# Kernel tuning notes

Hardware: AMD Instinct MI355X
Metric: run time of the kernel (lower is better)

Reference implementation:

```python
import jax, jax.numpy as jnp
import numpy as np


def setup_inputs() -> dict:
    key = jax.random.key(0)
    kK, kV, kQ, kP, kA = jax.random.split(key, 5)
    b, d, N, T = 16, 512, 1024, 2048
    K = jax.random.normal(kK, (b, d, N), dtype=jnp.float32)
    V = jax.random.normal(kV, (b, d, N), dtype=jnp.float32)
    Q = jax.random.normal(kQ, (b, d, T), dtype=jnp.float32)
    previous_position = jax.random.randint(kP, (b,), 0, N)
    # previous attention: a valid attention matrix (softmax over N)
    previous_att = jax.nn.softmax(jax.random.uniform(kA, (b, N, T), dtype=jnp.float32), axis=1)
    return {
        "K": K,
        "V": V,
        "Q": Q,
        "force_incremental": 1,   # static python int -> bool branch
        "previous_position": previous_position,
        "previous_att": previous_att,
        "current_time": 1024,     # static python int timestep
    }


def reference(K, V, Q, force_incremental, previous_position, previous_att, current_time):
    # K, V: [b, d, N]; Q: [b, d, T]
    d = Q.shape[1]
    scale = 1.0 / np.sqrt(d)  # Config.d == feature dim
    # A: [b, N, T], softmax over N (text axis)
    A = jax.nn.softmax(jnp.einsum('bdn,bdt->bnt', K, Q) * scale, axis=1)
    current_position = jnp.argmax(A[:, :, current_time], axis=1)  # [b]
    if force_incremental:
        N = A.shape[1]
        # restore already-committed alignment prefix
        A = A.at[:, :, :current_time].set(previous_att[:, :, :current_time])
        difference = current_position - previous_position
        force_needed = (difference < -1) | (difference > 3)  # [b]
        # delta: one-hot at previous_position+1 (scatter_ of ones collapses to one-hot)
        idx = jnp.clip(previous_position + 1, 0, N - 1)
        delta = jax.nn.one_hot(idx, N, dtype=A.dtype)  # [b, N]
        col = jnp.where(force_needed[:, None], delta, A[:, :, current_time])
        A = A.at[:, :, current_time].set(col)
        current_position = jnp.argmax(col, axis=1)
    # R: [b, d, T]
    R = jnp.einsum('bdn,bnt->bdt', V, A)
    return A, R, current_position
```

## Files before the change

kernel.cpp:

```cpp
#include <hip/hip_runtime.h>
#include <hip/hip_bf16.h>

#define B_  16
#define D_  512
#define N_  1024
#define T_  2048
#define CT_ 1024
#define SCALE 0.04419417382415922f

typedef __attribute__((ext_vector_type(8))) short bf16x8;
typedef __attribute__((ext_vector_type(4))) float f32x4;
typedef __attribute__((ext_vector_type(8))) unsigned short u16x8;

#define GLDS16(g, l) __builtin_amdgcn_global_load_lds( \
    (const __attribute__((address_space(1))) unsigned int*)(g), \
    (__attribute__((address_space(3))) unsigned int*)(l), 16, 0, 0)

__device__ __forceinline__ unsigned short f2bf(float f) {
    union { float f; unsigned u; } v; v.f = f;
    unsigned r = v.u + 0x7fffu + ((v.u >> 16) & 1u);
    return (unsigned short)(r >> 16);
}
__device__ __forceinline__ float bf2f(unsigned short s) {
    union { unsigned u; float f; } v; v.u = ((unsigned)s) << 16;
    return v.f;
}


__global__ __launch_bounds__(256) void prep_all(
    const float* __restrict__ K, const float* __restrict__ Q,
    const float* __restrict__ V, const float* __restrict__ prev_att,
    unsigned short* __restrict__ KT, unsigned short* __restrict__ QT,
    unsigned short* __restrict__ Vbf, float* __restrict__ A,
    unsigned short* __restrict__ PbfT, float* __restrict__ invsum,
    float* __restrict__ colS_part) {
    __shared__ float tl[64][65];
    __shared__ float qv_s[64];
    __shared__ float red[256];
    const int bid = blockIdx.x;
    const int tid = threadIdx.x;
    const int rr = tid >> 4, cc = (tid & 15) * 4;

    if (bid < 4096) {
        const int nx = bid & 15, rem = bid >> 4;
        const int ty_ = rem & 15, b = rem >> 4;
        const int n0 = nx * 64, t0 = ty_ * 64;
        const float* ib = prev_att + (long)b * N_ * T_;
        float* Ab = A + (long)b * N_ * T_;
        unsigned short* ob = PbfT + (long)b * T_ * N_;
        f32x4 v[4];
#pragma unroll
        for (int p = 0; p < 4; ++p)
            v[p] = __builtin_nontemporal_load(
                (const f32x4*)&ib[(long)(n0 + p * 16 + rr) * T_ + t0 + cc]);
#pragma unroll
        for (int p = 0; p < 4; ++p)
            __builtin_nontemporal_store(
                v[p], (f32x4*)&Ab[(long)(n0 + p * 16 + rr) * T_ + t0 + cc]);
#pragma unroll
        for (int p = 0; p < 4; ++p) {
            tl[p*16+rr][cc] = v[p][0]; tl[p*16+rr][cc+1] = v[p][1];
            tl[p*16+rr][cc+2] = v[p][2]; tl[p*16+rr][cc+3] = v[p][3];
        }
        __syncthreads();
#pragma unroll
        for (int p = 0; p < 4; ++p) {
            int c = p * 16 + rr;
            ushort4 w;
            w.x = f2bf(tl[cc+0][c]); w.y = f2bf(tl[cc+1][c]);
            w.z = f2bf(tl[cc+2][c]); w.w = f2bf(tl[cc+3][c]);
            *(ushort4*)&ob[(long)(t0 + c) * N_ + n0 + cc] = w;
        }
    } else if (bid < 6144) {
        const int r = bid - 4096;
        const int rx = r & 7, rem = r >> 3;
        const int cy = rem & 15, b = rem >> 4;
        const int r0 = rx * 64, c0 = cy * 64;
        const float* ib = K + (long)b * D_ * N_;
        unsigned short* ob = KT + (long)b * 1024 * 512;
        if (tid < 64)
            qv_s[tid] = __builtin_nontemporal_load(
                &Q[((long)b * D_ + r0 + tid) * T_ + CT_]);
        f32x4 v[4];
#pragma unroll
        for (int p = 0; p < 4; ++p)
            v[p] = __builtin_nontemporal_load(
                (const f32x4*)&ib[(long)(r0 + p * 16 + rr) * N_ + c0 + cc]);
#pragma unroll
        for (int p = 0; p < 4; ++p) {
            tl[p*16+rr][cc] = v[p][0]; tl[p*16+rr][cc+1] = v[p][1];
            tl[p*16+rr][cc+2] = v[p][2]; tl[p*16+rr][cc+3] = v[p][3];
        }
        __syncthreads();
#pragma unroll
        for (int p = 0; p < 4; ++p) {
            int c = p * 16 + rr;
            ushort4 w;
            w.x = f2bf(tl[cc+0][c]); w.y = f2bf(tl[cc+1][c]);
            w.z = f2bf(tl[cc+2][c]); w.w = f2bf(tl[cc+3][c]);
            *(ushort4*)&ob[(long)(c0 + c) * 512 + r0 + cc] = w;
        }
        {
            const int n = tid & 63, g = tid >> 6;
            float p = 0.f;
#pragma unroll
            for (int j = 0; j < 16; ++j)
                p += tl[g * 16 + j][n] * qv_s[g * 16 + j];
            red[tid] = p;
            __syncthreads();
            if (tid < 64)
                colS_part[((long)b * 8 + rx) * 1024 + c0 + tid] =
                    red[tid] + red[64 + tid] + red[128 + tid] + red[192 + tid];
        }
    } else if (bid < 8192) {
        const int r = bid - 6144;
        const int rx = r & 7, rem = r >> 3;
        const int cy = rem & 15, b = rem >> 4;
        const int r0 = rx * 64, c0 = cy * 64;
        const float* ib = Q + (long)b * D_ * T_;
        unsigned short* ob = QT + (long)b * 1024 * 512;
        f32x4 v[4];
#pragma unroll
        for (int p = 0; p < 4; ++p)
            v[p] = __builtin_nontemporal_load(
                (const f32x4*)&ib[(long)(r0 + p * 16 + rr) * T_ + CT_ + c0 + cc]);
#pragma unroll
        for (int p = 0; p < 4; ++p) {
            tl[p*16+rr][cc] = v[p][0]; tl[p*16+rr][cc+1] = v[p][1];
            tl[p*16+rr][cc+2] = v[p][2]; tl[p*16+rr][cc+3] = v[p][3];
        }
        __syncthreads();
#pragma unroll
        for (int p = 0; p < 4; ++p) {
            int c = p * 16 + rr;
            ushort4 w;
            w.x = f2bf(tl[cc+0][c]); w.y = f2bf(tl[cc+1][c]);
            w.z = f2bf(tl[cc+2][c]); w.w = f2bf(tl[cc+3][c]);
            *(ushort4*)&ob[(long)(c0 + c) * 512 + r0 + cc] = w;
        }
    } else if (bid < 9216) {
        const long total = (long)B_ * D_ * N_ / 4;
        for (long i = (long)(bid - 8192) * 256 + tid; i < total; i += 1024L * 256) {
            f32x4 v = __builtin_nontemporal_load(&((const f32x4*)V)[i]);
            ushort4 w;
            w.x = f2bf(v[0]); w.y = f2bf(v[1]); w.z = f2bf(v[2]); w.w = f2bf(v[3]);
            ((ushort4*)Vbf)[i] = w;
        }
    } else {
        const int idx = (bid - 9216) * 256 + tid;
        const int b = idx >> 10, t = idx & 1023;
        invsum[(long)b * T_ + t] = 1.0f;
    }
}

__global__ __launch_bounds__(256) void score_gemm_fused(
    const unsigned short* __restrict__ KT, const unsigned short* __restrict__ QT,
    unsigned short* __restrict__ PbfT, float* __restrict__ partial) {
    const int wg = blockIdx.x;
    const int b  = wg >> 6;
    const int rem = wg & 63;
    const int by = rem >> 3;
    const int bx = rem & 7;
    const int m0 = by * 128;
    const int t0 = bx * 128;
    __shared__ __align__(16) unsigned short buf[128 * 136];
    __shared__ float csum[2][128];
    unsigned short* sA = buf;
    unsigned short* sB = buf + 128 * 64;
    const int tid = threadIdx.x, lane = tid & 63, wave = tid >> 6;
    const int wm = wave >> 1, wn = wave & 1;
    const int lq = lane & 15, half = lane >> 4;
    const int srow = tid >> 3;
    const int cin  = tid & 7;

    const unsigned short* Ab = KT + (long)b * N_ * 512;
    const unsigned short* Bb = QT + (long)b * N_ * 512;

    f32x4 acc[4][4];
#pragma unroll
    for (int i = 0; i < 4; ++i)
#pragma unroll
        for (int j = 0; j < 4; ++j) acc[i][j] = f32x4{0.f, 0.f, 0.f, 0.f};

    for (int k0 = 0; k0 < 512; k0 += 64) {
#pragma unroll
        for (int c = 0; c < 4; ++c) {
            const int row  = c * 32 + srow;
            const int clog = cin ^ (row & 7);
            GLDS16(Ab + (long)(m0 + row) * 512 + k0 + clog * 8,
                   &sA[(c * 256 + wave * 64) * 8]);
            GLDS16(Bb + (long)(t0 + row) * 512 + k0 + clog * 8,
                   &sB[(c * 256 + wave * 64) * 8]);
        }
        __syncthreads();
#pragma unroll
        for (int kk = 0; kk < 2; ++kk) {
            bf16x8 af[4], bfr[4];
#pragma unroll
            for (int mi = 0; mi < 4; ++mi) {
                const int row = wm * 64 + mi * 16 + lq;
                af[mi] = *(const bf16x8*)&sA[row * 64 + (((kk * 4 + half) ^ (row & 7)) * 8)];
            }
#pragma unroll
            for (int ni = 0; ni < 4; ++ni) {
                const int row = wn * 64 + ni * 16 + lq;
                bfr[ni] = *(const bf16x8*)&sB[row * 64 + (((kk * 4 + half) ^ (row & 7)) * 8)];
            }
#pragma unroll
            for (int mi = 0; mi < 4; ++mi)
#pragma unroll
                for (int ni = 0; ni < 4; ++ni)
                    acc[mi][ni] = __builtin_amdgcn_mfma_f32_16x16x32_bf16(
                        af[mi], bfr[ni], acc[mi][ni], 0, 0, 0);
        }
        __syncthreads();
    }

#pragma unroll
    for (int mi = 0; mi < 4; ++mi)
#pragma unroll
        for (int ni = 0; ni < 4; ++ni)
#pragma unroll
            for (int r = 0; r < 4; ++r)
                acc[mi][ni][r] = __expf(acc[mi][ni][r] * SCALE);

    float cp[4];
#pragma unroll
    for (int ni = 0; ni < 4; ++ni) {
        float s = 0.f;
#pragma unroll
        for (int mi = 0; mi < 4; ++mi)
#pragma unroll
            for (int r = 0; r < 4; ++r) s += acc[mi][ni][r];
        s += __shfl_xor(s, 16);
        s += __shfl_xor(s, 32);
        cp[ni] = s;
    }

#pragma unroll
    for (int mi = 0; mi < 4; ++mi)
#pragma unroll
        for (int ni = 0; ni < 4; ++ni) {
            const int col = wn * 64 + ni * 16 + lq;
            const int row = wm * 64 + mi * 16 + half * 4;
            ushort4 w;
            w.x = f2bf(acc[mi][ni][0]); w.y = f2bf(acc[mi][ni][1]);
            w.z = f2bf(acc[mi][ni][2]); w.w = f2bf(acc[mi][ni][3]);
            *(ushort4*)&buf[col * 136 + row] = w;
        }
    if (lane < 16) {
#pragma unroll
        for (int ni = 0; ni < 4; ++ni)
            csum[wm][wn * 64 + ni * 16 + lane] = cp[ni];
    }
    __syncthreads();

    if (tid < 128)
        partial[((long)b * 8 + by) * 1024 + t0 + tid] =
            csum[0][tid] + csum[1][tid];

    unsigned short* ob = PbfT + (long)b * T_ * N_;
#pragma unroll
    for (int p = 0; p < 8; ++p) {
        const int idx = tid + p * 256;
        const int row = idx >> 4, ch = idx & 15;
        u16x8 w = *(const u16x8*)&buf[row * 136 + ch * 8];
        *(u16x8*)&ob[(long)(CT_ + t0 + row) * N_ + m0 + ch * 8] = w;
    }
}

__global__ void finalize_all(float* __restrict__ A, unsigned short* __restrict__ PbfT,
                             float* __restrict__ invsum,
                             const float* __restrict__ colS_part,
                             const float* __restrict__ partial,
                             float* __restrict__ pos_out,
                             const int* __restrict__ prev_pos,
                             const int* __restrict__ force_p) {
    const int force = *force_p;
    const int b = blockIdx.x;
    const int tid = threadIdx.x;
    float* Ab = A + (long)b * N_ * T_;
    __shared__ float s[N_];
    __shared__ float redf[256];
    __shared__ int   redi[256];

    for (int t = tid; t < 1024; t += 256) {
        float sm = 0.f;
#pragma unroll
        for (int k = 0; k < 8; ++k) sm += partial[((long)b * 8 + k) * 1024 + t];
        invsum[(long)b * T_ + CT_ + t] = 1.f / sm;
    }

    for (int n = tid; n < N_; n += 256) {
        float v = 0.f;
#pragma unroll
        for (int k = 0; k < 8; ++k) v += colS_part[((long)b * 8 + k) * 1024 + n];
        s[n] = v * SCALE;
    }
    __syncthreads();

    float m = -1e30f;
    for (int n = tid; n < N_; n += 256) m = fmaxf(m, s[n]);
    redf[tid] = m; __syncthreads();
    for (int w = 128; w > 0; w >>= 1) {
        if (tid < w) redf[tid] = fmaxf(redf[tid], redf[tid + w]);
        __syncthreads();
    }
    m = redf[0];
    __syncthreads();

    float sum = 0.f;
    for (int n = tid; n < N_; n += 256) sum += __expf(s[n] - m);
    redf[tid] = sum; __syncthreads();
    for (int w = 128; w > 0; w >>= 1) {
        if (tid < w) redf[tid] += redf[tid + w];
        __syncthreads();
    }
    sum = redf[0];
    __syncthreads();

    int idxl = N_;
    for (int n = tid; n < N_; n += 256) if (s[n] == m && n < idxl) idxl = n;
    redi[tid] = idxl; __syncthreads();
    for (int w = 128; w > 0; w >>= 1) {
        if (tid < w) redi[tid] = min(redi[tid], redi[tid + w]);
        __syncthreads();
    }
    const int cpos = redi[0];

    const int prev = prev_pos[b];
    const int diff = cpos - prev;
    const int fneed = force && (diff < -1 || diff > 3);
    int oneidx = prev + 1;
    oneidx = oneidx < 0 ? 0 : (oneidx > N_ - 1 ? N_ - 1 : oneidx);
    const float inv = 1.f / sum;

    for (int n = tid; n < N_; n += 256) {
        float v = fneed ? (n == oneidx ? 1.f : 0.f) : __expf(s[n] - m) * inv;
        Ab[(long)n * T_ + CT_] = v;
        PbfT[(long)b * T_ * N_ + (long)CT_ * N_ + n] = f2bf(v);
    }
    if (tid == 0) {
        invsum[(long)b * T_ + CT_] = 1.0f;
        pos_out[b] = (float)(fneed ? oneidx : cpos);
    }
}

__global__ __launch_bounds__(256) void rgemm_emitA(
    const unsigned short* __restrict__ Vbf, const unsigned short* __restrict__ PbfT,
    const float* __restrict__ invsum, float* __restrict__ R, float* __restrict__ A) {
    __shared__ __align__(16) unsigned char smem[33792];
    const int tid = threadIdx.x;

    if (blockIdx.x < 1024) {
        unsigned short* sA = (unsigned short*)smem;
        unsigned short* sB = (unsigned short*)(smem + 16384);
        const int wg = blockIdx.x;
        const int b  = wg >> 6;
        const int rem = wg & 63;
        const int by = rem >> 4;
        const int bx = rem & 15;
        const int m0  = by * 128;
        const int nn0 = bx * 128;
        const int lane = tid & 63, wave = tid >> 6;
        const int wm = wave >> 1, wn = wave & 1;
        const int lq = lane & 15, half = lane >> 4;
        const int srow = tid >> 3;
        const int cin  = tid & 7;

        const unsigned short* Ab = Vbf  + (long)b * D_ * N_;
        const unsigned short* Bb = PbfT + (long)b * T_ * N_;

        f32x4 acc[4][4];
#pragma unroll
        for (int i = 0; i < 4; ++i)
#pragma unroll
            for (int j = 0; j < 4; ++j) acc[i][j] = f32x4{0.f, 0.f, 0.f, 0.f};

        for (int k0 = 0; k0 < 1024; k0 += 64) {
#pragma unroll
            for (int c = 0; c < 4; ++c) {
                const int row  = c * 32 + srow;
                const int clog = cin ^ (row & 7);
                GLDS16(Ab + (long)(m0  + row) * 1024 + k0 + clog * 8,
                       &sA[(c * 256 + wave * 64) * 8]);
                GLDS16(Bb + (long)(nn0 + row) * 1024 + k0 + clog * 8,
                       &sB[(c * 256 + wave * 64) * 8]);
            }
            __syncthreads();
#pragma unroll
            for (int kk = 0; kk < 2; ++kk) {
                bf16x8 af[4], bfr[4];
#pragma unroll
                for (int mi = 0; mi < 4; ++mi) {
                    const int row = wm * 64 + mi * 16 + lq;
                    af[mi] = *(const bf16x8*)&sA[row * 64 + (((kk * 4 + half) ^ (row & 7)) * 8)];
                }
#pragma unroll
                for (int ni = 0; ni < 4; ++ni) {
                    const int row = wn * 64 + ni * 16 + lq;
                    bfr[ni] = *(const bf16x8*)&sB[row * 64 + (((kk * 4 + half) ^ (row & 7)) * 8)];
                }
#pragma unroll
                for (int mi = 0; mi < 4; ++mi)
#pragma unroll
                    for (int ni = 0; ni < 4; ++ni)
                        acc[mi][ni] = __builtin_amdgcn_mfma_f32_16x16x32_bf16(
                            af[mi], bfr[ni], acc[mi][ni], 0, 0, 0);
            }
            __syncthreads();
        }
        float* Rb = R + (long)b * D_ * T_;
#pragma unroll
        for (int ni = 0; ni < 4; ++ni) {
            const int col = nn0 + wn * 64 + ni * 16 + lq;
            const float inv = invsum[(long)b * T_ + col];
#pragma unroll
            for (int mi = 0; mi < 4; ++mi)
#pragma unroll
                for (int r = 0; r < 4; ++r) {
                    const int row = m0 + wm * 64 + mi * 16 + half * 4 + r;
                    __builtin_nontemporal_store(acc[mi][ni][r] * inv,
                                                &Rb[(long)row * T_ + col]);
                }
        }
    } else {
        float (*tl)[65] = (float(*)[65])smem;
        float* inv_s = (float*)(smem + 33280);
        const int r = blockIdx.x - 1024;
        const int n0x = r & 15, rem = r >> 4;
        const int tcy = rem & 7, b = rem >> 3;
        const int n0  = n0x * 64;
        const int tc0 = tcy * 128;
        if (tid < 128) inv_s[tid] = invsum[(long)b * T_ + CT_ + tc0 + tid];
        __syncthreads();
        const unsigned short* Pb = PbfT + (long)b * T_ * N_;
        float* Ab = A + (long)b * N_ * T_;
        const int rr = tid >> 4, cc = (tid & 15) * 4;
#pragma unroll
        for (int p = 0; p < 8; ++p) {
            const int row = p * 16 + rr;
            ushort4 w = *(const ushort4*)&Pb[(long)(CT_ + tc0 + row) * N_ + n0 + cc];
            const float inv = inv_s[row];
            tl[row][cc]   = bf2f(w.x) * inv; tl[row][cc+1] = bf2f(w.y) * inv;
            tl[row][cc+2] = bf2f(w.z) * inv; tl[row][cc+3] = bf2f(w.w) * inv;
        }
        __syncthreads();
        const int rr2 = tid >> 5, cc2 = (tid & 31) * 4;
#pragma unroll
        for (int p = 0; p < 8; ++p) {
            const int c = p * 8 + rr2;
            f32x4 o;
            o[0] = tl[cc2+0][c]; o[1] = tl[cc2+1][c];
            o[2] = tl[cc2+2][c]; o[3] = tl[cc2+3][c];
            __builtin_nontemporal_store(
                o, (f32x4*)&Ab[(long)(n0 + c) * T_ + CT_ + tc0 + cc2]);
        }
    }
}

__global__ void copy_prefix(const float* __restrict__ prev_att, float* __restrict__ A) {
    const int per_row = CT_ >> 2;
    const long total = (long)B_ * N_ * per_row;
    for (long i = (long)blockIdx.x * blockDim.x + threadIdx.x; i < total;
         i += (long)gridDim.x * blockDim.x) {
        long row = i / per_row;
        int  c4  = (int)(i - row * per_row);
        long off = row * T_ + (long)c4 * 4;
        *(float4*)(A + off) = *(const float4*)(prev_att + off);
    }
}

__global__ void softmax_part_old(const float* __restrict__ A, float* __restrict__ partial) {
    const int b  = blockIdx.z;
    const int n0 = blockIdx.y * 128;
    const int tx = threadIdx.x & 63, ty = threadIdx.x >> 6;
    const int ci = blockIdx.x * 64 + tx;
    const int t  = CT_ + ci;
    const float* Ab = A + (long)b * N_ * T_;
    float s = 0.f;
    for (int r = ty; r < 128; r += 4)
        s += __expf(Ab[(long)(n0 + r) * T_ + t] * SCALE);
    __shared__ float red2[4][64];
    red2[ty][tx] = s;
    __syncthreads();
    if (ty == 0) {
        float tot = red2[0][tx] + red2[1][tx] + red2[2][tx] + red2[3][tx];
        partial[((long)b * 8 + blockIdx.y) * 1024 + ci] = tot;
    }
}

__global__ __launch_bounds__(256) void score_gemm_old(
    const float* __restrict__ K, const float* __restrict__ Q, float* __restrict__ A) {
    const int b  = blockIdx.z;
    const int n0 = blockIdx.y * 128;
    const int t0 = blockIdx.x * 128;
    __shared__ __align__(16) unsigned short sK[128 * 40];
    __shared__ __align__(16) unsigned short sQ[128 * 40];
    const int tid = threadIdx.x;
    const int lane = tid & 63, wave = tid >> 6;
    const int wm = wave >> 1, wn = wave & 1;
    const int lq = lane & 15, half = lane >> 4;
    const int xl = tid & 127, grp = tid >> 7;
    f32x4 acc[4][4];
#pragma unroll
    for (int i = 0; i < 4; ++i)
#pragma unroll
        for (int j = 0; j < 4; ++j) acc[i][j] = f32x4{0.f, 0.f, 0.f, 0.f};
    const float* Kb = K + (long)b * D_ * N_;
    const float* Qb = Q + (long)b * D_ * T_;
    for (int d0 = 0; d0 < D_; d0 += 32) {
#pragma unroll
        for (int j = 0; j < 4; ++j) {
            ushort4 w;
#pragma unroll
            for (int i = 0; i < 4; ++i)
                ((unsigned short*)&w)[i] = f2bf(Kb[(long)(d0 + grp*16 + j*4 + i) * N_ + n0 + xl]);
            *(ushort4*)&sK[xl * 40 + grp * 16 + j * 4] = w;
        }
#pragma unroll
        for (int j = 0; j < 4; ++j) {
            ushort4 w;
#pragma unroll
            for (int i = 0; i < 4; ++i)
                ((unsigned short*)&w)[i] = f2bf(Qb[(long)(d0 + grp*16 + j*4 + i) * T_ + CT_ + t0 + xl]);
            *(ushort4*)&sQ[xl * 40 + grp * 16 + j * 4] = w;
        }
        __syncthreads();
        bf16x8 af[4], bfr[4];
#pragma unroll
        for (int mi = 0; mi < 4; ++mi)
            af[mi] = *(const bf16x8*)&sK[(wm * 64 + mi * 16 + lq) * 40 + half * 8];
#pragma unroll
        for (int ni = 0; ni < 4; ++ni)
            bfr[ni] = *(const bf16x8*)&sQ[(wn * 64 + ni * 16 + lq) * 40 + half * 8];
#pragma unroll
        for (int mi = 0; mi < 4; ++mi)
#pragma unroll
            for (int ni = 0; ni < 4; ++ni)
                acc[mi][ni] = __builtin_amdgcn_mfma_f32_16x16x32_bf16(
                    af[mi], bfr[ni], acc[mi][ni], 0, 0, 0);
        __syncthreads();
    }
    float* Ab = A + (long)b * N_ * T_;
#pragma unroll
    for (int mi = 0; mi < 4; ++mi)
#pragma unroll
        for (int ni = 0; ni < 4; ++ni) {
            const int col = CT_ + t0 + wn * 64 + ni * 16 + lq;
#pragma unroll
            for (int r = 0; r < 4; ++r)
                Ab[(long)(n0 + wm*64 + mi*16 + half*4 + r) * T_ + col] = acc[mi][ni][r];
        }
}

__global__ void softmax_scale_old(float* __restrict__ A, const float* __restrict__ partial) {
    const int b  = blockIdx.z;
    const int n0 = blockIdx.y * 256;
    const int tx = threadIdx.x & 63, ty = threadIdx.x >> 6;
    const int ci = blockIdx.x * 64 + tx;
    const int t  = CT_ + ci;
    float sum = 0.f;
#pragma unroll
    for (int k = 0; k < 8; ++k) sum += partial[((long)b * 8 + k) * 1024 + ci];
    const float inv = 1.f / sum;
    float* Ab = A + (long)b * N_ * T_;
    for (int r = ty; r < 256; r += 4) {
        long off = (long)(n0 + r) * T_ + t;
        Ab[off] = __expf(Ab[off] * SCALE) * inv;
    }
}

__global__ void col_scores_fp32(const float* __restrict__ K, const float* __restrict__ Q,
                                float* __restrict__ A) {
    const int b  = blockIdx.y;
    const int n0 = blockIdx.x * 128;
    const int tid = threadIdx.x;
    const int nl = tid & 127, dh = tid >> 7;
    __shared__ float qv[D_];
    __shared__ float part[256];
    for (int d = tid; d < D_; d += 256) qv[d] = Q[((long)b * D_ + d) * T_ + CT_];
    __syncthreads();
    float acc = 0.f;
    const float* Kb = K + (long)b * D_ * N_;
    for (int d = dh * 256; d < dh * 256 + 256; ++d)
        acc += Kb[(long)d * N_ + n0 + nl] * qv[d];
    part[tid] = acc;
    __syncthreads();
    if (tid < 128) {
        float s = (part[tid] + part[tid + 128]) * SCALE;
        A[((long)b * N_ + n0 + nl) * T_ + CT_] = s;
    }
}

__global__ void finalize_col_old(float* __restrict__ A, float* __restrict__ pos_out,
                                 const int* __restrict__ prev_pos,
                                 const int* __restrict__ force_p) {
    const int force = *force_p;
    const int b = blockIdx.x;
    const int tid = threadIdx.x;
    float* Ab = A + (long)b * N_ * T_;
    __shared__ float s[N_];
    __shared__ float redf[256];
    __shared__ int   redi[256];

    for (int n = tid; n < N_; n += 256) s[n] = Ab[(long)n * T_ + CT_];
    __syncthreads();
    float m = -1e30f;
    for (int n = tid; n < N_; n += 256) m = fmaxf(m, s[n]);
    redf[tid] = m; __syncthreads();
    for (int w = 128; w > 0; w >>= 1) {
        if (tid < w) redf[tid] = fmaxf(redf[tid], redf[tid + w]);
        __syncthreads();
    }
    m = redf[0];
    __syncthreads();
    float sum = 0.f;
    for (int n = tid; n < N_; n += 256) sum += __expf(s[n] - m);
    redf[tid] = sum; __syncthreads();
    for (int w = 128; w > 0; w >>= 1) {
        if (tid < w) redf[tid] += redf[tid + w];
        __syncthreads();
    }
    sum = redf[0];
    __syncthreads();
    int idxl = N_;
    for (int n = tid; n < N_; n += 256) if (s[n] == m && n < idxl) idxl = n;
    redi[tid] = idxl; __syncthreads();
    for (int w = 128; w > 0; w >>= 1) {
        if (tid < w) redi[tid] = min(redi[tid], redi[tid + w]);
        __syncthreads();
    }
    const int cpos = redi[0];
    const int prev = prev_pos[b];
    const int diff = cpos - prev;
    const int fneed = force && (diff < -1 || diff > 3);
    int oneidx = prev + 1;
    oneidx = oneidx < 0 ? 0 : (oneidx > N_ - 1 ? N_ - 1 : oneidx);
    const float inv = 1.f / sum;
    for (int n = tid; n < N_; n += 256) {
        float v = fneed ? (n == oneidx ? 1.f : 0.f) : __expf(s[n] - m) * inv;
        Ab[(long)n * T_ + CT_] = v;
    }
    if (tid == 0) pos_out[b] = (float)(fneed ? oneidx : cpos);
}

__global__ __launch_bounds__(256) void r_gemm_old(
    const float* __restrict__ V, const float* __restrict__ A, float* __restrict__ R) {
    const int b  = blockIdx.z;
    const int d0 = blockIdx.y * 128;
    const int t0 = blockIdx.x * 128;
    __shared__ __align__(16) unsigned short sV[128 * 40];
    __shared__ __align__(16) unsigned short sA2[128 * 40];
    const int tid = threadIdx.x;
    const int lane = tid & 63, wave = tid >> 6;
    const int wm = wave >> 1, wn = wave & 1;
    const int lq = lane & 15, half = lane >> 4;
    const int xl = tid & 127, grp = tid >> 7;
    const int vd = tid >> 3, vn4 = (tid & 7) * 4;
    f32x4 acc[4][4];
#pragma unroll
    for (int i = 0; i < 4; ++i)
#pragma unroll
        for (int j = 0; j < 4; ++j) acc[i][j] = f32x4{0.f, 0.f, 0.f, 0.f};
    const float* Vb = V + (long)b * D_ * N_;
    const float* Ab = A + (long)b * N_ * T_;
    for (int n0 = 0; n0 < N_; n0 += 32) {
#pragma unroll
        for (int p = 0; p < 4; ++p) {
            int dl = p * 32 + vd;
            float4 v = *(const float4*)&Vb[(long)(d0 + dl) * N_ + n0 + vn4];
            ushort4 w;
            w.x = f2bf(v.x); w.y = f2bf(v.y); w.z = f2bf(v.z); w.w = f2bf(v.w);
            *(ushort4*)&sV[dl * 40 + vn4] = w;
        }
#pragma unroll
        for (int j = 0; j < 4; ++j) {
            ushort4 w;
#pragma unroll
            for (int i = 0; i < 4; ++i)
                ((unsigned short*)&w)[i] = f2bf(Ab[(long)(n0 + grp*16 + j*4 + i) * T_ + t0 + xl]);
            *(ushort4*)&sA2[xl * 40 + grp * 16 + j * 4] = w;
        }
        __syncthreads();
        bf16x8 af[4], bfr[4];
#pragma unroll
        for (int mi = 0; mi < 4; ++mi)
            af[mi] = *(const bf16x8*)&sV[(wm * 64 + mi * 16 + lq) * 40 + half * 8];
#pragma unroll
        for (int ni = 0; ni < 4; ++ni)
            bfr[ni] = *(const bf16x8*)&sA2[(wn * 64 + ni * 16 + lq) * 40 + half * 8];
#pragma unroll
        for (int mi = 0; mi < 4; ++mi)
#pragma unroll
            for (int ni = 0; ni < 4; ++ni)
                acc[mi][ni] = __builtin_amdgcn_mfma_f32_16x16x32_bf16(
                    af[mi], bfr[ni], acc[mi][ni], 0, 0, 0);
        __syncthreads();
    }
    float* Rb = R + (long)b * D_ * T_;
#pragma unroll
    for (int mi = 0; mi < 4; ++mi)
#pragma unroll
        for (int ni = 0; ni < 4; ++ni) {
            const int col = t0 + wn * 64 + ni * 16 + lq;
#pragma unroll
            for (int r = 0; r < 4; ++r)
                Rb[(long)(d0 + wm*64 + mi*16 + half*4 + r) * T_ + col] = acc[mi][ni][r];
        }
}

extern "C" void kernel_launch(void* const* d_in, const int* in_sizes, int n_in,
                              void* d_out, int out_size, void* d_ws, size_t ws_size,
                              hipStream_t stream) {
    const float* K        = (const float*)d_in[0];
    const float* V        = (const float*)d_in[1];
    const float* Q        = (const float*)d_in[2];
    const int*   force_p  = (const int*)d_in[3];
    const int*   prev_pos = (const int*)d_in[4];
    const float* prev_att = (const float*)d_in[5];

    float* A       = (float*)d_out;
    float* R       = A + (long)B_ * N_ * T_;
    float* pos_out = R + (long)B_ * D_ * T_;

    const size_t oKT = 0;
    const size_t oQT = oKT + (size_t)B_ * N_ * D_ * 2;
    const size_t oV  = oQT + (size_t)B_ * N_ * D_ * 2;
    const size_t oPT = oV  + (size_t)B_ * D_ * N_ * 2;
    const size_t oP  = oPT + (size_t)B_ * T_ * N_ * 2;
    const size_t oI  = oP  + (size_t)B_ * 8 * 1024 * 4;
    const size_t oCP = oI  + (size_t)B_ * T_ * 4;
    const size_t need = oCP + (size_t)B_ * 8 * 1024 * 4;

    float* partial = (float*)((char*)d_ws + (ws_size >= need ? oP : 0));

    if (ws_size >= need) {
        unsigned short* KT   = (unsigned short*)((char*)d_ws + oKT);
        unsigned short* QT   = (unsigned short*)((char*)d_ws + oQT);
        unsigned short* Vbf  = (unsigned short*)((char*)d_ws + oV);
        unsigned short* PbfT = (unsigned short*)((char*)d_ws + oPT);
        float*          invs = (float*)((char*)d_ws + oI);
        float*          colP = (float*)((char*)d_ws + oCP);

        prep_all        <<<9280, 256, 0, stream>>>(K, Q, V, prev_att,
                                                   KT, QT, Vbf, A, PbfT, invs, colP);
        score_gemm_fused<<<1024, 256, 0, stream>>>(KT, QT, PbfT, partial);
        finalize_all    <<<B_, 256, 0, stream>>>(A, PbfT, invs, colP, partial,
                                                 pos_out, prev_pos, force_p);
        rgemm_emitA     <<<3072, 256, 0, stream>>>(Vbf, PbfT, invs, R, A);
    } else {
        copy_prefix       <<<2048, 256, 0, stream>>>(prev_att, A);
        score_gemm_old    <<<dim3(8, 8, B_), 256, 0, stream>>>(K, Q, A);
        softmax_part_old  <<<dim3(16, 8, B_), 256, 0, stream>>>(A, partial);
        softmax_scale_old <<<dim3(16, 4, B_), 256, 0, stream>>>(A, partial);
        col_scores_fp32   <<<dim3(8, B_), 256, 0, stream>>>(K, Q, A);
        finalize_col_old  <<<B_, 256, 0, stream>>>(A, pos_out, prev_pos, force_p);
        r_gemm_old        <<<dim3(16, 4, B_), 256, 0, stream>>>(V, A, R);
    }
}
```

Measured before the change: 164.5 us.

## Interleave score GEMM blocks with prefix copy and V conversion in one launch

Moves the previous-attention prefix copy/transposition and the V-to-bf16 conversion out of the prep kernel and into the score GEMM launch. Every sixth block does the GEMM and the rest do the memory-bound copy work, so compute-heavy and bandwidth-heavy blocks can run on the GPU at the same time. The prep kernel is reduced to the K/Q transpose and init. The cost is more shared memory per block for the copy blocks (sized for the GEMM) and possible contention on memory bandwidth while the GEMM blocks are running.

New measurement: 179.6 us. 9.2% more time.

```diff
diff --git a/kernel.cpp b/kernel.cpp
--- a/kernel.cpp
+++ b/kernel.cpp
@@ -27,13 +27,10 @@
 }
 
 
-__global__ __launch_bounds__(256) void prep_all(
+__global__ __launch_bounds__(256) void prep_kq(
     const float* __restrict__ K, const float* __restrict__ Q,
-    const float* __restrict__ V, const float* __restrict__ prev_att,
     unsigned short* __restrict__ KT, unsigned short* __restrict__ QT,
-    unsigned short* __restrict__ Vbf, float* __restrict__ A,
-    unsigned short* __restrict__ PbfT, float* __restrict__ invsum,
-    float* __restrict__ colS_part) {
+    float* __restrict__ invsum, float* __restrict__ colS_part) {
     __shared__ float tl[64][65];
     __shared__ float qv_s[64];
     __shared__ float red[256];
@@ -41,39 +38,8 @@
     const int tid = threadIdx.x;
     const int rr = tid >> 4, cc = (tid & 15) * 4;
 
-    if (bid < 4096) {
-        const int nx = bid & 15, rem = bid >> 4;
-        const int ty_ = rem & 15, b = rem >> 4;
-        const int n0 = nx * 64, t0 = ty_ * 64;
-        const float* ib = prev_att + (long)b * N_ * T_;
-        float* Ab = A + (long)b * N_ * T_;
-        unsigned short* ob = PbfT + (long)b * T_ * N_;
-        f32x4 v[4];
-#pragma unroll
-        for (int p = 0; p < 4; ++p)
-            v[p] = __builtin_nontemporal_load(
-                (const f32x4*)&ib[(long)(n0 + p * 16 + rr) * T_ + t0 + cc]);
-#pragma unroll
-        for (int p = 0; p < 4; ++p)
-            __builtin_nontemporal_store(
-                v[p], (f32x4*)&Ab[(long)(n0 + p * 16 + rr) * T_ + t0 + cc]);
-#pragma unroll
-        for (int p = 0; p < 4; ++p) {
-            tl[p*16+rr][cc] = v[p][0]; tl[p*16+rr][cc+1] = v[p][1];
-            tl[p*16+rr][cc+2] = v[p][2]; tl[p*16+rr][cc+3] = v[p][3];
-        }
-        __syncthreads();
-#pragma unroll
-        for (int p = 0; p < 4; ++p) {
-            int c = p * 16 + rr;
-            ushort4 w;
-            w.x = f2bf(tl[cc+0][c]); w.y = f2bf(tl[cc+1][c]);
-            w.z = f2bf(tl[cc+2][c]); w.w = f2bf(tl[cc+3][c]);
-            *(ushort4*)&ob[(long)(t0 + c) * N_ + n0 + cc] = w;
-        }
-    } else if (bid < 6144) {
-        const int r = bid - 4096;
-        const int rx = r & 7, rem = r >> 3;
+    if (bid < 2048) {
+        const int rx = bid & 7, rem = bid >> 3;
         const int cy = rem & 15, b = rem >> 4;
         const int r0 = rx * 64, c0 = cy * 64;
         const float* ib = K + (long)b * D_ * N_;
@@ -112,8 +78,8 @@
                 colS_part[((long)b * 8 + rx) * 1024 + c0 + tid] =
                     red[tid] + red[64 + tid] + red[128 + tid] + red[192 + tid];
         }
-    } else if (bid < 8192) {
-        const int r = bid - 6144;
+    } else if (bid < 4096) {
+        const int r = bid - 2048;
         const int rx = r & 7, rem = r >> 3;
         const int cy = rem & 15, b = rem >> 4;
         const int r0 = rx * 64, c0 = cy * 64;
@@ -138,134 +104,177 @@
             w.z = f2bf(tl[cc+2][c]); w.w = f2bf(tl[cc+3][c]);
             *(ushort4*)&ob[(long)(c0 + c) * 512 + r0 + cc] = w;
         }
-    } else if (bid < 9216) {
-        const long total = (long)B_ * D_ * N_ / 4;
-        for (long i = (long)(bid - 8192) * 256 + tid; i < total; i += 1024L * 256) {
-            f32x4 v = __builtin_nontemporal_load(&((const f32x4*)V)[i]);
-            ushort4 w;
-            w.x = f2bf(v[0]); w.y = f2bf(v[1]); w.z = f2bf(v[2]); w.w = f2bf(v[3]);
-            ((ushort4*)Vbf)[i] = w;
-        }
     } else {
-        const int idx = (bid - 9216) * 256 + tid;
+        const int idx = (bid - 4096) * 256 + tid;
         const int b = idx >> 10, t = idx & 1023;
         invsum[(long)b * T_ + t] = 1.0f;
     }
 }
 
-__global__ __launch_bounds__(256) void score_gemm_fused(
+__global__ __launch_bounds__(256) void score_prefix_v(
     const unsigned short* __restrict__ KT, const unsigned short* __restrict__ QT,
-    unsigned short* __restrict__ PbfT, float* __restrict__ partial) {
-    const int wg = blockIdx.x;
-    const int b  = wg >> 6;
-    const int rem = wg & 63;
-    const int by = rem >> 3;
-    const int bx = rem & 7;
-    const int m0 = by * 128;
-    const int t0 = bx * 128;
-    __shared__ __align__(16) unsigned short buf[128 * 136];
-    __shared__ float csum[2][128];
-    unsigned short* sA = buf;
-    unsigned short* sB = buf + 128 * 64;
-    const int tid = threadIdx.x, lane = tid & 63, wave = tid >> 6;
-    const int wm = wave >> 1, wn = wave & 1;
-    const int lq = lane & 15, half = lane >> 4;
-    const int srow = tid >> 3;
-    const int cin  = tid & 7;
-
-    const unsigned short* Ab = KT + (long)b * N_ * 512;
-    const unsigned short* Bb = QT + (long)b * N_ * 512;
-
-    f32x4 acc[4][4];
-#pragma unroll
-    for (int i = 0; i < 4; ++i)
-#pragma unroll
-        for (int j = 0; j < 4; ++j) acc[i][j] = f32x4{0.f, 0.f, 0.f, 0.f};
-
-    for (int k0 = 0; k0 < 512; k0 += 64) {
-#pragma unroll
-        for (int c = 0; c < 4; ++c) {
-            const int row  = c * 32 + srow;
-            const int clog = cin ^ (row & 7);
-            GLDS16(Ab + (long)(m0 + row) * 512 + k0 + clog * 8,
-                   &sA[(c * 256 + wave * 64) * 8]);
-            GLDS16(Bb + (long)(t0 + row) * 512 + k0 + clog * 8,
-                   &sB[(c * 256 + wave * 64) * 8]);
-        }
-        __syncthreads();
-#pragma unroll
-        for (int kk = 0; kk < 2; ++kk) {
-            bf16x8 af[4], bfr[4];
-#pragma unroll
-            for (int mi = 0; mi < 4; ++mi) {
-                const int row = wm * 64 + mi * 16 + lq;
-                af[mi] = *(const bf16x8*)&sA[row * 64 + (((kk * 4 + half) ^ (row & 7)) * 8)];
+    const float* __restrict__ prev_att, const float* __restrict__ V,
+    unsigned short* __restrict__ PbfT, float* __restrict__ partial,
+    float* __restrict__ A, unsigned short* __restrict__ Vbf) {
+    __shared__ __align__(16) unsigned char smem[35840];
+    const int bid = blockIdx.x;
+    const int tid = threadIdx.x;
+
+    if (bid % 6 == 0) {
+        unsigned short* buf = (unsigned short*)smem;
+        float (*csum)[128]  = (float(*)[128])(smem + 34816);
+        unsigned short* sA = buf;
+        unsigned short* sB = buf + 128 * 64;
+        const int wg = bid / 6;
+        const int b  = wg >> 6;
+        const int rem = wg & 63;
+        const int by = rem >> 3;
+        const int bx = rem & 7;
+        const int m0 = by * 128;
+        const int t0 = bx * 128;
+        const int lane = tid & 63, wave = tid >> 6;
+        const int wm = wave >> 1, wn = wave & 1;
+        const int lq = lane & 15, half = lane >> 4;
+        const int srow = tid >> 3;
+        const int cin  = tid & 7;
+
+        const unsigned short* Ab = KT + (long)b * N_ * 512;
+        const unsigned short* Bb = QT + (long)b * N_ * 512;
+
+        f32x4 acc[4][4];
+#pragma unroll
+        for (int i = 0; i < 4; ++i)
+#pragma unroll
+            for (int j = 0; j < 4; ++j) acc[i][j] = f32x4{0.f, 0.f, 0.f, 0.f};
+
+        for (int k0 = 0; k0 < 512; k0 += 64) {
+#pragma unroll
+            for (int c = 0; c < 4; ++c) {
+                const int row  = c * 32 + srow;
+                const int clog = cin ^ (row & 7);
+                GLDS16(Ab + (long)(m0 + row) * 512 + k0 + clog * 8,
+                       &sA[(c * 256 + wave * 64) * 8]);
+                GLDS16(Bb + (long)(t0 + row) * 512 + k0 + clog * 8,
+                       &sB[(c * 256 + wave * 64) * 8]);
             }
+            __syncthreads();
+#pragma unroll
+            for (int kk = 0; kk < 2; ++kk) {
+                bf16x8 af[4], bfr[4];
+#pragma unroll
+                for (int mi = 0; mi < 4; ++mi) {
+                    const int row = wm * 64 + mi * 16 + lq;
+                    af[mi] = *(const bf16x8*)&sA[row * 64 + (((kk * 4 + half) ^ (row & 7)) * 8)];
+                }
+#pragma unroll
+                for (int ni = 0; ni < 4; ++ni) {
+                    const int row = wn * 64 + ni * 16 + lq;
+                    bfr[ni] = *(const bf16x8*)&sB[row * 64 + (((kk * 4 + half) ^ (row & 7)) * 8)];
+                }
+#pragma unroll
+                for (int mi = 0; mi < 4; ++mi)
+#pragma unroll
+                    for (int ni = 0; ni < 4; ++ni)
+                        acc[mi][ni] = __builtin_amdgcn_mfma_f32_16x16x32_bf16(
+                            af[mi], bfr[ni], acc[mi][ni], 0, 0, 0);
+            }
+            __syncthreads();
+        }
+
+#pragma unroll
+        for (int mi = 0; mi < 4; ++mi)
+#pragma unroll
+            for (int ni = 0; ni < 4; ++ni)
+#pragma unroll
+                for (int r = 0; r < 4; ++r)
+                    acc[mi][ni][r] = __expf(acc[mi][ni][r] * SCALE);
+
+        float cp[4];
+#pragma unroll
+        for (int ni = 0; ni < 4; ++ni) {
+            float s = 0.f;
+#pragma unroll
+            for (int mi = 0; mi < 4; ++mi)
+#pragma unroll
+                for (int r = 0; r < 4; ++r) s += acc[mi][ni][r];
+            s += __shfl_xor(s, 16);
+            s += __shfl_xor(s, 32);
+            cp[ni] = s;
+        }
+
+#pragma unroll
+        for (int mi = 0; mi < 4; ++mi)
 #pragma unroll
             for (int ni = 0; ni < 4; ++ni) {
-                const int row = wn * 64 + ni * 16 + lq;
-                bfr[ni] = *(const bf16x8*)&sB[row * 64 + (((kk * 4 + half) ^ (row & 7)) * 8)];
+                const int col = wn * 64 + ni * 16 + lq;
+                const int row = wm * 64 + mi * 16 + half * 4;
+                ushort4 w;
+                w.x = f2bf(acc[mi][ni][0]); w.y = f2bf(acc[mi][ni][1]);
+                w.z = f2bf(acc[mi][ni][2]); w.w = f2bf(acc[mi][ni][3]);
+                *(ushort4*)&buf[col * 136 + row] = w;
             }
-#pragma unroll
-            for (int mi = 0; mi < 4; ++mi)
-#pragma unroll
-                for (int ni = 0; ni < 4; ++ni)
-                    acc[mi][ni] = __builtin_amdgcn_mfma_f32_16x16x32_bf16(
-                        af[mi], bfr[ni], acc[mi][ni], 0, 0, 0);
-        }
-        __syncthreads();
-    }
-
-#pragma unroll
-    for (int mi = 0; mi < 4; ++mi)
-#pragma unroll
-        for (int ni = 0; ni < 4; ++ni)
-#pragma unroll
-            for (int r = 0; r < 4; ++r)
-                acc[mi][ni][r] = __expf(acc[mi][ni][r] * SCALE);
-
-    float cp[4];
-#pragma unroll
-    for (int ni = 0; ni < 4; ++ni) {
-        float s = 0.f;
-#pragma unroll
-        for (int mi = 0; mi < 4; ++mi)
-#pragma unroll
-            for (int r = 0; r < 4; ++r) s += acc[mi][ni][r];
-        s += __shfl_xor(s, 16);
-        s += __shfl_xor(s, 32);
-        cp[ni] = s;
-    }
-
-#pragma unroll
-    for (int mi = 0; mi < 4; ++mi)
-#pragma unroll
-        for (int ni = 0; ni < 4; ++ni) {
-            const int col = wn * 64 + ni * 16 + lq;
-            const int row = wm * 64 + mi * 16 + half * 4;
-            ushort4 w;
-            w.x = f2bf(acc[mi][ni][0]); w.y = f2bf(acc[mi][ni][1]);
-            w.z = f2bf(acc[mi][ni][2]); w.w = f2bf(acc[mi][ni][3]);
-            *(ushort4*)&buf[col * 136 + row] = w;
-        }
-    if (lane < 16) {
-#pragma unroll
-        for (int ni = 0; ni < 4; ++ni)
-            csum[wm][wn * 64 + ni * 16 + lane] = cp[ni];
-    }
-    __syncthreads();
-
-    if (tid < 128)
-        partial[((long)b * 8 + by) * 1024 + t0 + tid] =
-            csum[0][tid] + csum[1][tid];
-
-    unsigned short* ob = PbfT + (long)b * T_ * N_;
-#pragma unroll
-    for (int p = 0; p < 8; ++p) {
-        const int idx = tid + p * 256;
-        const int row = idx >> 4, ch = idx & 15;
-        u16x8 w = *(const u16x8*)&buf[row * 136 + ch * 8];
-        *(u16x8*)&ob[(long)(CT_ + t0 + row) * N_ + m0 + ch * 8] = w;
+        if (lane < 16) {
+#pragma unroll
+            for (int ni = 0; ni < 4; ++ni)
+                csum[wm][wn * 64 + ni * 16 + lane] = cp[ni];
+        }
+        __syncthreads();
+
+        if (tid < 128)
+            partial[((long)b * 8 + by) * 1024 + t0 + tid] =
+                csum[0][tid] + csum[1][tid];
+
+        unsigned short* ob = PbfT + (long)b * T_ * N_;
+#pragma unroll
+        for (int p = 0; p < 8; ++p) {
+            const int idx = tid + p * 256;
+            const int row = idx >> 4, ch = idx & 15;
+            u16x8 w = *(const u16x8*)&buf[row * 136 + ch * 8];
+            *(u16x8*)&ob[(long)(CT_ + t0 + row) * N_ + m0 + ch * 8] = w;
+        }
+    } else {
+        const int oid = bid - bid / 6 - 1;
+        if (oid < 4096) {
+            float (*tl)[65] = (float(*)[65])smem;
+            const int rr = tid >> 4, cc = (tid & 15) * 4;
+            const int nx = oid & 15, rem = oid >> 4;
+            const int ty_ = rem & 15, b = rem >> 4;
+            const int n0 = nx * 64, t0 = ty_ * 64;
+            const float* ib = prev_att + (long)b * N_ * T_;
+            float* Ab = A + (long)b * N_ * T_;
+            unsigned short* ob = PbfT + (long)b * T_ * N_;
+            f32x4 v[4];
+#pragma unroll
+            for (int p = 0; p < 4; ++p)
+                v[p] = __builtin_nontemporal_load(
+                    (const f32x4*)&ib[(long)(n0 + p * 16 + rr) * T_ + t0 + cc]);
+#pragma unroll
+            for (int p = 0; p < 4; ++p)
+                __builtin_nontemporal_store(
+                    v[p], (f32x4*)&Ab[(long)(n0 + p * 16 + rr) * T_ + t0 + cc]);
+#pragma unroll
+            for (int p = 0; p < 4; ++p) {
+                tl[p*16+rr][cc] = v[p][0]; tl[p*16+rr][cc+1] = v[p][1];
+                tl[p*16+rr][cc+2] = v[p][2]; tl[p*16+rr][cc+3] = v[p][3];
+            }
+            __syncthreads();
+#pragma unroll
+            for (int p = 0; p < 4; ++p) {
+                int c = p * 16 + rr;
+                ushort4 w;
+                w.x = f2bf(tl[cc+0][c]); w.y = f2bf(tl[cc+1][c]);
+                w.z = f2bf(tl[cc+2][c]); w.w = f2bf(tl[cc+3][c]);
+                *(ushort4*)&ob[(long)(t0 + c) * N_ + n0 + cc] = w;
+            }
+        } else {
+            const long total = (long)B_ * D_ * N_ / 4;
+            for (long i = (long)(oid - 4096) * 256 + tid; i < total; i += 1024L * 256) {
+                f32x4 v = __builtin_nontemporal_load(&((const f32x4*)V)[i]);
+                ushort4 w;
+                w.x = f2bf(v[0]); w.y = f2bf(v[1]); w.z = f2bf(v[2]); w.w = f2bf(v[3]);
+                ((ushort4*)Vbf)[i] = w;
+            }
+        }
     }
 }
 
@@ -743,12 +752,12 @@
         float*          invs = (float*)((char*)d_ws + oI);
         float*          colP = (float*)((char*)d_ws + oCP);
 
-        prep_all        <<<9280, 256, 0, stream>>>(K, Q, V, prev_att,
-                                                   KT, QT, Vbf, A, PbfT, invs, colP);
-        score_gemm_fused<<<1024, 256, 0, stream>>>(KT, QT, PbfT, partial);
-        finalize_all    <<<B_, 256, 0, stream>>>(A, PbfT, invs, colP, partial,
-                                                 pos_out, prev_pos, force_p);
-        rgemm_emitA     <<<3072, 256, 0, stream>>>(Vbf, PbfT, invs, R, A);
+        prep_kq        <<<4160, 256, 0, stream>>>(K, Q, KT, QT, invs, colP);
+        score_prefix_v <<<6144, 256, 0, stream>>>(KT, QT, prev_att, V,
+                                                  PbfT, partial, A, Vbf);
+        finalize_all   <<<B_, 256, 0, stream>>>(A, PbfT, invs, colP, partial,
+                                                pos_out, prev_pos, force_p);
+        rgemm_emitA    <<<3072, 256, 0, stream>>>(Vbf, PbfT, invs, R, A);
     } else {
         copy_prefix       <<<2048, 256, 0, stream>>>(prev_att, A);
         score_gemm_old    <<<dim3(8, 8, B_), 256, 0, stream>>>(K, Q, A);
```
